# Kernel optimization log

Measured on AMD Instinct MI355X. Metric: run time of the kernel, lower is better.

The kernel has to match this reference:

```python
import jax, jax.numpy as jnp
import numpy as np

B, S, D, H = 4, 2048, 1024, 16
DK = D // H
INFTY = 1000000.0
INIT_SCALE = 1.2  # RandomUniform(-1.2, 1.2) kernel initializer


def setup_inputs() -> dict:
    key = jax.random.key(0)
    ks = jax.random.split(key, 6)
    x = jax.random.normal(ks[0], (B, S, D), dtype=jnp.float32)
    mask = jax.random.randint(ks[1], (B, S), 0, 2) == 1  # bool padding mask
    WQ = jax.random.uniform(ks[2], (D, D), jnp.float32, -INIT_SCALE, INIT_SCALE)
    WK = jax.random.uniform(ks[3], (D, D), jnp.float32, -INIT_SCALE, INIT_SCALE)
    WV = jax.random.uniform(ks[4], (D, D), jnp.float32, -INIT_SCALE, INIT_SCALE)
    WO = jax.random.uniform(ks[5], (D, D), jnp.float32, -INIT_SCALE, INIT_SCALE)
    return {"x": x, "mask": mask, "WQ": WQ, "WK": WK, "WV": WV, "WO": WO}


def reference(x, mask, WQ, WK, WV, WO):
    # Faithful reproduction of the layout: reshape to (B, S, d_key, n_heads)
    # then permute, matching K.reshape/K.permute_dimensions in the original.
    q = (x @ WQ).reshape(B, S, DK, H).transpose(0, 3, 1, 2)  # (B, H, S, DK)
    k = (x @ WK).reshape(B, S, DK, H).transpose(0, 3, 2, 1)  # (B, H, DK, S)
    score = jnp.matmul(q, k) / np.sqrt(DK)                   # (B, H, S, S)
    # additive key masking: score - (~mask)[B,1,1,S] * infinity
    inv_mask = (~mask).astype(x.dtype)
    score = score - inv_mask[:, None, None, :] * INFTY
    score = jax.nn.softmax(score, axis=-1)                   # att_dropout == 0
    v = (x @ WV).reshape(B, S, DK, H).transpose(0, 3, 1, 2)  # (B, H, S, DK)
    o = jnp.matmul(score, v)                                 # (B, H, S, DK)
    o = o.transpose(0, 2, 1, 3).reshape(B, S, H * DK)
    o = o @ WO                                               # (B, S, D)
    # final query-position masking + abs, as in the original
    o = jnp.abs(o * mask.astype(x.dtype)[:, :, None])
    return o
```

## Files before the change

### kernel.cpp

```cpp
#include <hip/hip_runtime.h>
#include <hip/hip_bf16.h>
#include <cstdint>
#include <cstddef>

constexpr int Bc  = 4;
constexpr int Sc  = 2048;
constexpr int Dc  = 1024;
constexpr int Hc  = 16;
constexpr int DKc = 64;
constexpr int Mtot = Bc * Sc;
constexpr float SC2  = 0.125f * 1.4426950408889634f;
constexpr float INF2 = 1000000.0f * 1.4426950408889634f;
constexpr float SXq  = 5400.0f;
constexpr float SWq  = 27166.0f;
constexpr float INVS = 1.0f / (SXq * SWq);

typedef short bf16x8 __attribute__((ext_vector_type(8)));
typedef float f32x4  __attribute__((ext_vector_type(4)));
typedef int   i32x4  __attribute__((ext_vector_type(4)));
typedef unsigned int u32x4 __attribute__((ext_vector_type(4)));

__device__ inline unsigned short bf16_rn(float f) {
    uint32_t u = __float_as_uint(f);
    uint32_t r = (u + 0x7FFFu + ((u >> 16) & 1u)) >> 16;
    return (unsigned short)r;
}
__device__ inline uint32_t pk_bf16(float a, float b) {
    uint32_t d;
    asm("v_cvt_pk_bf16_f32 %0, %1, %2" : "=v"(d) : "v"(a), "v"(b));
    return d;
}
__device__ inline int perm64(int k) {
    return (k & ~63) | (((k & 15) << 2) | ((k >> 4) & 3));
}
__device__ inline void mfma_i8(i32x4& acc, u32x4 a, u32x4 b) {
    asm volatile("v_mfma_i32_16x16x64_i8 %0, %1, %2, %0" : "+v"(acc) : "v"(a), "v"(b));
}
__device__ inline void split_i16(int fx, char& h, char& l) {
    int lo = ((fx + 128) & 255) - 128;
    h = (char)((fx - lo) >> 8);
    l = (char)lo;
}
__device__ inline void gl_lds16(const void* g, void* l) {
    __builtin_amdgcn_global_load_lds(
        (const __attribute__((address_space(1))) unsigned int*)g,
        (__attribute__((address_space(3))) unsigned int*)l, 16, 0, 0);
}

__global__ __launch_bounds__(256) void mask_norm(const void* __restrict__ mraw,
                                                 int* __restrict__ mi,
                                                 int* __restrict__ rinv,
                                                 int* __restrict__ nbv,
                                                 int* __restrict__ npadv) {
    __shared__ int fF32, fU8, fI32;
    __shared__ int part[256];
    __shared__ int nb_sh;
    if (threadIdx.x == 0) { fF32 = 0; fU8 = 0; fI32 = 0; }
    __syncthreads();
    const unsigned char* mb = (const unsigned char*)mraw;
    int aF = 0, a1 = 0, a4 = 0;
    for (int i = threadIdx.x; i < Mtot; i += 256) {
        unsigned char v = mb[i];
        if ((i & 3) == 3 && v == 0x3F) aF = 1;
        if (v) {
            if (i & 3) a1 = 1;
            else if (i & 7) a4 = 1;
        }
    }
    if (aF) fF32 = 1;
    if (a1) fU8 = 1;
    if (a4) fI32 = 1;
    __syncthreads();
    if (fF32) {
        const float* mf = (const float*)mraw;
        for (int s = threadIdx.x; s < Mtot; s += 256) mi[s] = (mf[s] != 0.0f);
    } else if (fU8) {
        for (int s = threadIdx.x; s < Mtot; s += 256) mi[s] = (mb[s] != 0);
    } else if (fI32) {
        const int* m32 = (const int*)mraw;
        for (int s = threadIdx.x; s < Mtot; s += 256) mi[s] = (m32[s] != 0);
    } else {
        const long long* m64 = (const long long*)mraw;
        for (int s = threadIdx.x; s < Mtot; s += 256) mi[s] = (m64[s] != 0);
    }
    __syncthreads();

    for (int b = 0; b < Bc; ++b) {
        const int* mrow = mi + b * Sc;
        int loc[8], cnt = 0;
        #pragma unroll
        for (int u = 0; u < 8; ++u) {
            loc[u] = mrow[threadIdx.x * 8 + u];
            cnt += loc[u];
        }
        part[threadIdx.x] = cnt;
        __syncthreads();
        if (threadIdx.x == 0) {
            int run = 0;
            for (int i = 0; i < 256; ++i) { int c = part[i]; part[i] = run; run += c; }
            nbv[b] = run;
            npadv[b] = (run + 63) & ~63;
            nb_sh = run;
        }
        __syncthreads();
        const int nbb = nb_sh;
        int pos = part[threadIdx.x];
        #pragma unroll
        for (int u = 0; u < 8; ++u) {
            const int s = threadIdx.x * 8 + u;
            if (loc[u]) {
                rinv[b * Sc + pos] = s;
                pos++;
            } else {
                rinv[b * Sc + nbb + (s - pos)] = s;
            }
        }
        __syncthreads();
    }
}

__global__ __launch_bounds__(256) void zero_pad(const int* __restrict__ nbv,
                                                const int* __restrict__ npadv,
                                                unsigned short* __restrict__ Khi,
                                                unsigned short* __restrict__ Klo,
                                                unsigned short* __restrict__ Vt) {
    const int bh = blockIdx.x;
    const int b = bh >> 4;
    const int nb = nbv[b], np = npadv[b];
    const int t = threadIdx.x;
    const size_t kbase = (size_t)bh * Sc * DKc;
    const size_t vbase = (size_t)bh * DKc * Sc;
    const int n = (np - nb) * DKc;
    for (int i = t; i < n; i += 256) {
        const int r = nb + i / DKc, c = i % DKc;
        Khi[kbase + (size_t)r * DKc + c] = 0;
        Klo[kbase + (size_t)r * DKc + c] = 0;
        Vt[vbase + (size_t)c * Sc + perm64(r)] = 0;
    }
}

__global__ __launch_bounds__(256) void quant_x(const float* __restrict__ x,
                                               unsigned short* __restrict__ xhi,
                                               signed char* __restrict__ xh8,
                                               signed char* __restrict__ xl8) {
    const int i = (blockIdx.x * 256 + threadIdx.x) * 4;
    float4 v = *reinterpret_cast<const float4*>(x + i);
    ushort4 hb;
    hb.x = bf16_rn(v.x); hb.y = bf16_rn(v.y); hb.z = bf16_rn(v.z); hb.w = bf16_rn(v.w);
    *reinterpret_cast<ushort4*>(xhi + i) = hb;
    char4 h8, l8;
    int fx;
    fx = min(max(__float2int_rn(v.x * SXq), -32640), 32640); split_i16(fx, h8.x, l8.x);
    fx = min(max(__float2int_rn(v.y * SXq), -32640), 32640); split_i16(fx, h8.y, l8.y);
    fx = min(max(__float2int_rn(v.z * SXq), -32640), 32640); split_i16(fx, h8.z, l8.z);
    fx = min(max(__float2int_rn(v.w * SXq), -32640), 32640); split_i16(fx, h8.w, l8.w);
    *reinterpret_cast<char4*>(xh8 + i) = h8;
    *reinterpret_cast<char4*>(xl8 + i) = l8;
}

template<bool PERM>
__global__ __launch_bounds__(256) void split_wt(const float* __restrict__ W,
                                                unsigned short* __restrict__ WhT) {
    __shared__ float ls[64][68];
    const int k0 = blockIdx.y * 64, n0 = blockIdx.x * 64;
    const int t = threadIdx.x;
    #pragma unroll
    for (int l = 0; l < 4; ++l) {
        const int idx = t + l * 256;
        const int r = idx >> 4, c = (idx & 15) * 4;
        *reinterpret_cast<float4*>(&ls[r][c]) =
            *reinterpret_cast<const float4*>(W + (size_t)(k0 + r) * Dc + n0 + c);
    }
    __syncthreads();
    #pragma unroll
    for (int l = 0; l < 4; ++l) {
        const int idx = t + l * 256;
        const int on = idx >> 4, kq = (idx & 15) * 4;
        #pragma unroll
        for (int j = 0; j < 4; ++j) {
            const float v = ls[kq + j][on];
            const int k  = k0 + kq + j;
            const int kd = PERM ? perm64(k) : k;
            WhT[(size_t)(n0 + on) * Dc + kd] = bf16_rn(v);
        }
    }
}

__global__ __launch_bounds__(256) void split_wt_i8(const float* __restrict__ W,
                                                   signed char* __restrict__ Wh8,
                                                   signed char* __restrict__ Wl8) {
    __shared__ float ls[64][68];
    const int k0 = blockIdx.y * 64, n0 = blockIdx.x * 64;
    const int t = threadIdx.x;
    #pragma unroll
    for (int l = 0; l < 4; ++l) {
        const int idx = t + l * 256;
        const int r = idx >> 4, c = (idx & 15) * 4;
        *reinterpret_cast<float4*>(&ls[r][c]) =
            *reinterpret_cast<const float4*>(W + (size_t)(k0 + r) * Dc + n0 + c);
    }
    __syncthreads();
    #pragma unroll
    for (int l = 0; l < 4; ++l) {
        const int idx = t + l * 256;
        const int on = idx >> 4, kq = (idx & 15) * 4;
        char4 hv, lv;
        int fx;
        fx = __float2int_rn(ls[kq + 0][on] * SWq); split_i16(fx, hv.x, lv.x);
        fx = __float2int_rn(ls[kq + 1][on] * SWq); split_i16(fx, hv.y, lv.y);
        fx = __float2int_rn(ls[kq + 2][on] * SWq); split_i16(fx, hv.z, lv.z);
        fx = __float2int_rn(ls[kq + 3][on] * SWq); split_i16(fx, hv.w, lv.w);
        const size_t o = (size_t)(n0 + on) * Dc + k0 + kq;
        *reinterpret_cast<char4*>(Wh8 + o) = hv;
        *reinterpret_cast<char4*>(Wl8 + o) = lv;
    }
}

__global__ __launch_bounds__(256) void gemm_i8qk(
    const signed char* __restrict__ Ah8, const signed char* __restrict__ Al8,
    const signed char* __restrict__ Bh8, const signed char* __restrict__ Bl8,
    const int* __restrict__ rinv, const int* __restrict__ nbv, float scale,
    unsigned short* __restrict__ O1, unsigned short* __restrict__ O2) {
    __shared__ __align__(16) signed char Ah[128 * 64];
    __shared__ __align__(16) signed char Al[128 * 64];
    __shared__ __align__(16) signed char Bh[128 * 64];
    __shared__ __align__(16) signed char Bl[128 * 64];
    const int t = threadIdx.x;
    const int n0 = blockIdx.x * 128, m0 = blockIdx.y * 128;
    const int b = m0 >> 11, mm0 = m0 & 2047;
    const int nb = nbv[b];
    if (mm0 >= nb) return;
    const int wv = t >> 6, lane = t & 63, li = lane & 15, lg = lane >> 4;
    const int wm = (wv >> 1) * 64, wn = (wv & 1) * 64;

    size_t gAr[2];
    int rowN[2];
    #pragma unroll
    for (int c = 0; c < 2; ++c) {
        const int ci  = wv * 2 + c;
        const int row = ci * 16 + (lane >> 2);
        rowN[c] = n0 + row;
        gAr[c] = ((size_t)b * Sc + rinv[b * Sc + mm0 + row]) * Dc;
    }
    const int cq = (lane & 3) * 16;

    i32x4 a1[4][4] = {};
    i32x4 a2[4][4] = {};
    asm volatile("s_nop 7" :::);

    for (int k0 = 0; k0 < Dc; k0 += 64) {
        __syncthreads();
        #pragma unroll
        for (int c = 0; c < 2; ++c) {
            const int ci = wv * 2 + c;
            const size_t ga = gAr[c] + k0 + cq;
            const size_t gb = (size_t)rowN[c] * Dc + k0 + cq;
            gl_lds16(Ah8 + ga, &Ah[ci * 1024]);
            gl_lds16(Al8 + ga, &Al[ci * 1024]);
            gl_lds16(Bh8 + gb, &Bh[ci * 1024]);
            gl_lds16(Bl8 + gb, &Bl[ci * 1024]);
        }
        __syncthreads();

        u32x4 bhf[4], blf[4];
        #pragma unroll
        for (int ni = 0; ni < 4; ++ni) {
            bhf[ni] = *reinterpret_cast<const u32x4*>(&Bh[(wn + ni * 16 + li) * 64 + lg * 16]);
            blf[ni] = *reinterpret_cast<const u32x4*>(&Bl[(wn + ni * 16 + li) * 64 + lg * 16]);
        }
        #pragma unroll
        for (int mi = 0; mi < 4; ++mi) {
            const u32x4 ahf = *reinterpret_cast<const u32x4*>(&Ah[(wm + mi * 16 + li) * 64 + lg * 16]);
            const u32x4 alf = *reinterpret_cast<const u32x4*>(&Al[(wm + mi * 16 + li) * 64 + lg * 16]);
            #pragma unroll
            for (int ni = 0; ni < 4; ++ni) {
                mfma_i8(a1[mi][ni], ahf, bhf[ni]);
                mfma_i8(a2[mi][ni], ahf, blf[ni]);
                mfma_i8(a2[mi][ni], alf, bhf[ni]);
            }
        }
    }

    asm volatile("s_nop 7\ns_nop 7\ns_nop 7" :::);

    #pragma unroll
    for (int mi = 0; mi < 4; ++mi) {
        #pragma unroll
        for (int r = 0; r < 4; ++r) {
            const int cs = mm0 + wm + mi * 16 + lg * 4 + r;
            if (cs >= nb) continue;
            #pragma unroll
            for (int ni = 0; ni < 4; ++ni) {
                const int n = n0 + wn + ni * 16 + li;
                const int h = n & 15, dk = n >> 4;
                const float f = fmaf((float)a1[mi][ni][r], 65536.0f,
                                     (float)a2[mi][ni][r] * 256.0f) * scale;
                const size_t o = ((size_t)(b * Hc + h) * Sc + cs) * DKc + dk;
                const unsigned short hi = bf16_rn(f);
                O1[o] = hi;
                O2[o] = bf16_rn(f - __uint_as_float((uint32_t)hi << 16));
            }
        }
    }
}

template<int EPI>
__global__ __launch_bounds__(256) void gemm_bf16(
    const unsigned short* __restrict__ Ahi,
    const unsigned short* __restrict__ Bhi,
    const int* __restrict__ rinv, const int* __restrict__ nbv,
    unsigned short* __restrict__ O1,
    float* __restrict__ Of) {
    __shared__ __align__(16) unsigned short Ah[128 * 32];
    __shared__ __align__(16) unsigned short Bh[128 * 32];
    const int t = threadIdx.x;
    const int n0 = blockIdx.x * 128, m0 = blockIdx.y * 128;
    const int b = m0 >> 11, mm0 = m0 & 2047;
    const int nb = nbv[b];
    const int wv = t >> 6, lane = t & 63, li = lane & 15, lg = lane >> 4;
    const int wm = (wv >> 1) * 64, wn = (wv & 1) * 64;

    if (EPI == 1 && mm0 >= nb) return;
    if (EPI == 2 && mm0 >= nb) {
        #pragma unroll
        for (int mi = 0; mi < 4; ++mi) {
            #pragma unroll
            for (int r = 0; r < 4; ++r) {
                const int cs = mm0 + wm + mi * 16 + lg * 4 + r;
                const int gs = rinv[b * Sc + cs];
                #pragma unroll
                for (int ni = 0; ni < 4; ++ni) {
                    const int n = n0 + wn + ni * 16 + li;
                    Of[((size_t)(b * Sc + gs)) * Dc + n] = 0.0f;
                }
            }
        }
        return;
    }

    size_t gAr[2];
    int rowN[2];
    #pragma unroll
    for (int c = 0; c < 2; ++c) {
        const int ci  = wv * 2 + c;
        const int row = ci * 16 + (lane >> 2);
        rowN[c] = n0 + row;
        if (EPI == 1)
            gAr[c] = ((size_t)b * Sc + rinv[b * Sc + mm0 + row]) * Dc;
        else
            gAr[c] = (size_t)(m0 + row) * Dc;
    }
    const int cq = (lane & 3) * 8;

    f32x4 acc[4][4] = {};

    for (int k0 = 0; k0 < Dc; k0 += 32) {
        __syncthreads();
        #pragma unroll
        for (int c = 0; c < 2; ++c) {
            const int ci = wv * 2 + c;
            gl_lds16(Ahi + gAr[c] + k0 + cq, &Ah[ci * 512]);
            gl_lds16(Bhi + (size_t)rowN[c] * Dc + k0 + cq, &Bh[ci * 512]);
        }
        __syncthreads();

        bf16x8 bhf[4];
        #pragma unroll
        for (int ni = 0; ni < 4; ++ni)
            bhf[ni] = *reinterpret_cast<const bf16x8*>(&Bh[(wn + ni * 16 + li) * 32 + lg * 8]);
        #pragma unroll
        for (int mi = 0; mi < 4; ++mi) {
            const bf16x8 ahf = *reinterpret_cast<const bf16x8*>(&Ah[(wm + mi * 16 + li) * 32 + lg * 8]);
            #pragma unroll
            for (int ni = 0; ni < 4; ++ni)
                acc[mi][ni] = __builtin_amdgcn_mfma_f32_16x16x32_bf16(ahf, bhf[ni], acc[mi][ni], 0, 0, 0);
        }
    }

    #pragma unroll
    for (int mi = 0; mi < 4; ++mi) {
        #pragma unroll
        for (int r = 0; r < 4; ++r) {
            const int cs = mm0 + wm + mi * 16 + lg * 4 + r;
            if (EPI == 1) {
                if (cs >= nb) continue;
                #pragma unroll
                for (int ni = 0; ni < 4; ++ni) {
                    const int n = n0 + wn + ni * 16 + li;
                    const int h = n & 15, dk = n >> 4;
                    O1[((size_t)(b * Hc + h) * DKc + dk) * Sc + perm64(cs)] =
                        bf16_rn(acc[mi][ni][r]);
                }
            } else {
                const int gs = rinv[b * Sc + cs];
                const bool valid = (cs < nb);
                #pragma unroll
                for (int ni = 0; ni < 4; ++ni) {
                    const int n = n0 + wn + ni * 16 + li;
                    Of[((size_t)(b * Sc + gs)) * Dc + n] =
                        valid ? fabsf(acc[mi][ni][r]) : 0.0f;
                }
            }
        }
    }
}

__global__ __launch_bounds__(512) void attn_mfma(const unsigned short* __restrict__ Qhi,
                                                 const unsigned short* __restrict__ Qlo,
                                                 const unsigned short* __restrict__ Khi,
                                                 const unsigned short* __restrict__ Klo,
                                                 const unsigned short* __restrict__ Vtg,
                                                 const int* __restrict__ nbv,
                                                 const int* __restrict__ npadv,
                                                 unsigned short* __restrict__ att) {
    constexpr int TK = 64;
    const int id  = blockIdx.x;
    const int swz = (id & 7) * 128 + (id >> 3);
    const int qb  = swz & 15;
    const int bh  = swz >> 4;
    const int b = bh >> 4, h = bh & 15;
    const int q0 = qb * 128;
    const int nb = nbv[b];
    if (q0 >= nb) return;
    const int ntile = npadv[b] >> 6;
    const int nt2 = (ntile + 1) >> 1;

    __shared__ __align__(16) unsigned short PsKs[2][128][72];
    __shared__ __align__(16) unsigned short Vs[2][80][72];

    const int t    = threadIdx.x;
    const int grp  = t >> 8;
    const int tg   = t & 255;
    const int wave = tg >> 6;
    const int lane = t & 63;
    const int lg   = lane >> 4;
    const int li   = lane & 15;

    const int myBase = grp ? nt2 : 0;
    const int myEnd  = grp ? ntile : nt2;

    {
        const int r = 64 + (tg >> 4), c4 = (tg & 15) * 4;
        const unsigned short val = ((tg >> 4) == 0) ? (unsigned short)0x3F80 : (unsigned short)0;
        ushort4 v; v.x = val; v.y = val; v.z = val; v.w = val;
        *reinterpret_cast<ushort4*>(&Vs[grp][r][c4]) = v;
    }

    bf16x8 qh[2][2], ql[2][2];
    #pragma unroll
    for (int hf = 0; hf < 2; ++hf) {
        const size_t qrow = ((size_t)bh * Sc + q0 + wave * 32 + hf * 16 + li) * DKc + lg * 8;
        qh[hf][0] = *reinterpret_cast<const bf16x8*>(Qhi + qrow);
        qh[hf][1] = *reinterpret_cast<const bf16x8*>(Qhi + qrow + 32);
        ql[hf][0] = *reinterpret_cast<const bf16x8*>(Qlo + qrow);
        ql[hf][1] = *reinterpret_cast<const bf16x8*>(Qlo + qrow + 32);
    }

    const size_t kbase = (size_t)bh * Sc * DKc;
    const size_t vbase = (size_t)bh * DKc * Sc;

    f32x4 accO[2][5] = {};
    float m[2][4];
    #pragma unroll
    for (int hf = 0; hf < 2; ++hf)
        #pragma unroll
        for (int r = 0; r < 4; ++r) m[hf][r] = -1e30f;

    for (int it = 0; it < nt2; ++it) {
        const int kt = myBase + it;
        const bool act = (kt < myEnd);
        const int k0 = kt * TK;
        __syncthreads();
        if (act) {
            #pragma unroll
            for (int u = 0; u < 2; ++u) {
                const int idx = tg + u * 256;
                const int r = idx >> 3, cc = (idx & 7) * 8;
                *reinterpret_cast<uint4*>(&PsKs[grp][r][cc]) =
                    *reinterpret_cast<const uint4*>(Khi + kbase + (size_t)(k0 + r) * DKc + cc);
                *reinterpret_cast<uint4*>(&PsKs[grp][64 + r][cc]) =
                    *reinterpret_cast<const uint4*>(Klo + kbase + (size_t)(k0 + r) * DKc + cc);
                *reinterpret_cast<uint4*>(&Vs[grp][r][cc]) =
                    *reinterpret_cast<const uint4*>(Vtg + vbase + (size_t)r * Sc + k0 + cc);
            }
        }
        __syncthreads();
        if (!act) continue;

        float sc[2][4][4];
        #pragma unroll
        for (int n = 0; n < 4; ++n) {
            const bf16x8 kh0 = *reinterpret_cast<const bf16x8*>(&PsKs[grp][n * 16 + li][lg * 8]);
            const bf16x8 kh1 = *reinterpret_cast<const bf16x8*>(&PsKs[grp][n * 16 + li][32 + lg * 8]);
            const bf16x8 kl0 = *reinterpret_cast<const bf16x8*>(&PsKs[grp][64 + n * 16 + li][lg * 8]);
            const bf16x8 kl1 = *reinterpret_cast<const bf16x8*>(&PsKs[grp][64 + n * 16 + li][32 + lg * 8]);
            const float mz = (k0 + n * 16 + li < nb) ? 0.0f : INF2;
            #pragma unroll
            for (int hf = 0; hf < 2; ++hf) {
                f32x4 a = {0, 0, 0, 0};
                a = __builtin_amdgcn_mfma_f32_16x16x32_bf16(qh[hf][0], kh0, a, 0, 0, 0);
                a = __builtin_amdgcn_mfma_f32_16x16x32_bf16(qh[hf][1], kh1, a, 0, 0, 0);
                a = __builtin_amdgcn_mfma_f32_16x16x32_bf16(qh[hf][0], kl0, a, 0, 0, 0);
                a = __builtin_amdgcn_mfma_f32_16x16x32_bf16(qh[hf][1], kl1, a, 0, 0, 0);
                a = __builtin_amdgcn_mfma_f32_16x16x32_bf16(ql[hf][0], kh0, a, 0, 0, 0);
                a = __builtin_amdgcn_mfma_f32_16x16x32_bf16(ql[hf][1], kh1, a, 0, 0, 0);
                #pragma unroll
                for (int r = 0; r < 4; ++r) sc[hf][n][r] = a[r] - mz;
            }
        }

        float mx[2][4], rs[2][4];
        #pragma unroll
        for (int hf = 0; hf < 2; ++hf)
            #pragma unroll
            for (int r = 0; r < 4; ++r)
                mx[hf][r] = fmaxf(fmaxf(sc[hf][0][r], sc[hf][1][r]),
                                  fmaxf(sc[hf][2][r], sc[hf][3][r]));
        #pragma unroll
        for (int o = 1; o < 16; o <<= 1)
            #pragma unroll
            for (int hf = 0; hf < 2; ++hf)
                #pragma unroll
                for (int r = 0; r < 4; ++r)
                    mx[hf][r] = fmaxf(mx[hf][r], __shfl_xor(mx[hf][r], o));
        #pragma unroll
        for (int hf = 0; hf < 2; ++hf)
            #pragma unroll
            for (int r = 0; r < 4; ++r) {
                const float mn = fmaxf(m[hf][r], mx[hf][r]);
                rs[hf][r] = exp2f(m[hf][r] - mn);
                m[hf][r]  = mn;
            }
        #pragma unroll
        for (int hf = 0; hf < 2; ++hf)
            #pragma unroll
            for (int r = 0; r < 4; ++r) {
                const float p0 = exp2f(sc[hf][0][r] - m[hf][r]);
                const float p1 = exp2f(sc[hf][1][r] - m[hf][r]);
                const float p2 = exp2f(sc[hf][2][r] - m[hf][r]);
                const float p3 = exp2f(sc[hf][3][r] - m[hf][r]);
                uint2 w;
                w.x = pk_bf16(p0, p1);
                w.y = pk_bf16(p2, p3);
                *reinterpret_cast<uint2*>(&PsKs[grp][wave * 32 + hf * 16 + lg * 4 + r][li * 4]) = w;
            }

        #pragma unroll
        for (int hf = 0; hf < 2; ++hf)
            #pragma unroll
            for (int dt = 0; dt < 5; ++dt)
                #pragma unroll
                for (int r = 0; r < 4; ++r)
                    accO[hf][dt][r] *= rs[hf][r];

        #pragma unroll
        for (int c = 0; c < 2; ++c) {
            bf16x8 pa[2];
            #pragma unroll
            for (int hf = 0; hf < 2; ++hf)
                pa[hf] = *reinterpret_cast<const bf16x8*>(&PsKs[grp][wave * 32 + hf * 16 + li][c * 32 + lg * 8]);
            #pragma unroll
            for (int dt = 0; dt < 5; ++dt) {
                const bf16x8 vb = *reinterpret_cast<const bf16x8*>(&Vs[grp][dt * 16 + li][c * 32 + lg * 8]);
                #pragma unroll
                for (int hf = 0; hf < 2; ++hf)
                    accO[hf][dt] = __builtin_amdgcn_mfma_f32_16x16x32_bf16(pa[hf], vb, accO[hf][dt], 0, 0, 0);
            }
        }
    }

    __syncthreads();
    float* pO  = (float*)&PsKs[0][0][0];
    float* pML = pO + 128 * 64;

    if (grp == 1) {
        #pragma unroll
        for (int hf = 0; hf < 2; ++hf) {
            #pragma unroll
            for (int r = 0; r < 4; ++r) {
                const int row = wave * 32 + hf * 16 + lg * 4 + r;
                if (li == 0) {
                    pML[row * 2]     = m[hf][r];
                    pML[row * 2 + 1] = accO[hf][4][r];
                }
                float4 o = make_float4(accO[hf][0][r], accO[hf][1][r],
                                       accO[hf][2][r], accO[hf][3][r]);
                *reinterpret_cast<float4*>(&pO[row * 64 + li * 4]) = o;
            }
        }
    }
    __syncthreads();
    if (grp == 0) {
        #pragma unroll
        for (int hf = 0; hf < 2; ++hf) {
            #pragma unroll
            for (int r = 0; r < 4; ++r) {
                const int row = wave * 32 + hf * 16 + lg * 4 + r;
                const float m1 = pML[row * 2];
                const float l1 = pML[row * 2 + 1];
                const float l0 = __shfl(accO[hf][4][r], lane & 0x30);
                const float ms = fmaxf(m[hf][r], m1);
                const float s0 = exp2f(m[hf][r] - ms);
                const float s1 = exp2f(m1 - ms);
                const float inv = 1.0f / (l0 * s0 + l1 * s1);
                const float4 o1 = *reinterpret_cast<const float4*>(&pO[row * 64 + li * 4]);
                const int q = q0 + row;
                uint2 w;
                w.x = pk_bf16((accO[hf][0][r] * s0 + o1.x * s1) * inv,
                              (accO[hf][1][r] * s0 + o1.y * s1) * inv);
                w.y = pk_bf16((accO[hf][2][r] * s0 + o1.z * s1) * inv,
                              (accO[hf][3][r] * s0 + o1.w * s1) * inv);
                *reinterpret_cast<uint2*>(att + (size_t)(b * Sc + q) * Dc + h * DKc + li * 4) = w;
            }
        }
    }
}

extern "C" void kernel_launch(void* const* d_in, const int* in_sizes, int n_in,
                              void* d_out, int out_size, void* d_ws, size_t ws_size,
                              hipStream_t stream) {
    const float* x    = (const float*)d_in[0];
    const void*  mraw = d_in[1];
    const float* WQ   = (const float*)d_in[2];
    const float* WK   = (const float*)d_in[3];
    const float* WV   = (const float*)d_in[4];
    const float* WO   = (const float*)d_in[5];
    float* out = (float*)d_out;

    int* mi    = (int*)d_ws;
    int* rinv  = mi + Mtot;
    int* nbv   = rinv + Mtot;
    int* npadv = nbv + 4;
    const size_t SZ = (size_t)Mtot * Dc;
    const size_t WSZ = (size_t)Dc * Dc;
    char* p = (char*)d_ws + 65664;
    unsigned short* xhi = (unsigned short*)p;            p += SZ * 2;
    signed char*    xh8 = (signed char*)p;               p += SZ;
    signed char*    xl8 = (signed char*)p;               p += SZ;
    unsigned short* WVh = (unsigned short*)p;            p += WSZ * 2;
    unsigned short* WOh = (unsigned short*)p;            p += WSZ * 2;
    signed char*    WQh8 = (signed char*)p;              p += WSZ;
    signed char*    WQl8 = (signed char*)p;              p += WSZ;
    signed char*    WKh8 = (signed char*)p;              p += WSZ;
    signed char*    WKl8 = (signed char*)p;              p += WSZ;
    unsigned short* Qhi = (unsigned short*)p;            p += SZ * 2;
    unsigned short* Qlo = (unsigned short*)p;            p += SZ * 2;
    unsigned short* Khi = (unsigned short*)p;            p += SZ * 2;
    unsigned short* Klo = (unsigned short*)p;            p += SZ * 2;
    unsigned short* Vt  = (unsigned short*)p;            p += SZ * 2;
    unsigned short* att = xhi;

    mask_norm<<<1, 256, 0, stream>>>(mraw, mi, rinv, nbv, npadv);
    quant_x<<<(int)(SZ / 1024), 256, 0, stream>>>(x, xhi, xh8, xl8);
    const dim3 gW(16, 16);
    split_wt_i8<<<gW, 256, 0, stream>>>(WQ, WQh8, WQl8);
    split_wt_i8<<<gW, 256, 0, stream>>>(WK, WKh8, WKl8);
    split_wt<false><<<gW, 256, 0, stream>>>(WV, WVh);
    split_wt<true ><<<gW, 256, 0, stream>>>(WO, WOh);
    zero_pad<<<dim3(64), 256, 0, stream>>>(nbv, npadv, Khi, Klo, Vt);

    const dim3 gG(Dc / 128, Mtot / 128);
    gemm_i8qk<<<gG, 256, 0, stream>>>(xh8, xl8, WQh8, WQl8, rinv, nbv, SC2 * INVS, Qhi, Qlo);
    gemm_i8qk<<<gG, 256, 0, stream>>>(xh8, xl8, WKh8, WKl8, rinv, nbv, INVS, Khi, Klo);
    gemm_bf16<1><<<gG, 256, 0, stream>>>(xhi, WVh, rinv, nbv, Vt, nullptr);

    attn_mfma<<<dim3(1024), 512, 0, stream>>>(Qhi, Qlo, Khi, Klo, Vt, nbv, npadv, att);

    gemm_bf16<2><<<gG, 256, 0, stream>>>(att, WOh, rinv, nbv, nullptr, out);
}
```

Baseline: 305.5 us.

## Fuse Q, K, V projections into one int8 split-precision GEMM launch

The V projection moves from the bf16 GEMM to the same int8 hi/lo split GEMM used for Q and K. All three weight matrices are concatenated into one buffer and computed by a single launch with 24 column tiles, and each tile picks its output tensor and scale from its column range. This drops the bf16 copy of x, the separate bf16 V weight, and two kernel launches, and it gives better occupancy through one larger grid. In exchange V now costs three int8 MFMAs per step instead of one bf16 MFMA. The V epilogue also changes to the int8 scaling and rounding path.

After: 321.2 us. +5.1%, slower.

```diff
diff --git a/kernel.cpp b/kernel.cpp
--- a/kernel.cpp
+++ b/kernel.cpp
@@ -140,14 +140,10 @@
 }
 
 __global__ __launch_bounds__(256) void quant_x(const float* __restrict__ x,
-                                               unsigned short* __restrict__ xhi,
                                                signed char* __restrict__ xh8,
                                                signed char* __restrict__ xl8) {
     const int i = (blockIdx.x * 256 + threadIdx.x) * 4;
     float4 v = *reinterpret_cast<const float4*>(x + i);
-    ushort4 hb;
-    hb.x = bf16_rn(v.x); hb.y = bf16_rn(v.y); hb.z = bf16_rn(v.z); hb.w = bf16_rn(v.w);
-    *reinterpret_cast<ushort4*>(xhi + i) = hb;
     char4 h8, l8;
     int fx;
     fx = min(max(__float2int_rn(v.x * SXq), -32640), 32640); split_i16(fx, h8.x, l8.x);
@@ -158,9 +154,8 @@
     *reinterpret_cast<char4*>(xl8 + i) = l8;
 }
 
-template<bool PERM>
-__global__ __launch_bounds__(256) void split_wt(const float* __restrict__ W,
-                                                unsigned short* __restrict__ WhT) {
+__global__ __launch_bounds__(256) void split_wt_o(const float* __restrict__ W,
+                                                  unsigned short* __restrict__ WhT) {
     __shared__ float ls[64][68];
     const int k0 = blockIdx.y * 64, n0 = blockIdx.x * 64;
     const int t = threadIdx.x;
@@ -179,8 +174,7 @@
         #pragma unroll
         for (int j = 0; j < 4; ++j) {
             const float v = ls[kq + j][on];
-            const int k  = k0 + kq + j;
-            const int kd = PERM ? perm64(k) : k;
+            const int kd = perm64(k0 + kq + j);
             WhT[(size_t)(n0 + on) * Dc + kd] = bf16_rn(v);
         }
     }
@@ -216,11 +210,13 @@
     }
 }
 
-__global__ __launch_bounds__(256) void gemm_i8qk(
+__global__ __launch_bounds__(256) void gemm_i8qkv(
     const signed char* __restrict__ Ah8, const signed char* __restrict__ Al8,
     const signed char* __restrict__ Bh8, const signed char* __restrict__ Bl8,
-    const int* __restrict__ rinv, const int* __restrict__ nbv, float scale,
-    unsigned short* __restrict__ O1, unsigned short* __restrict__ O2) {
+    const int* __restrict__ rinv, const int* __restrict__ nbv,
+    unsigned short* __restrict__ Qhi, unsigned short* __restrict__ Qlo,
+    unsigned short* __restrict__ Khi, unsigned short* __restrict__ Klo,
+    unsigned short* __restrict__ Vt) {
     __shared__ __align__(16) signed char Ah[128 * 64];
     __shared__ __align__(16) signed char Al[128 * 64];
     __shared__ __align__(16) signed char Bh[128 * 64];
@@ -283,6 +279,11 @@
 
     asm volatile("s_nop 7\ns_nop 7\ns_nop 7" :::);
 
+    const int sel = n0 >> 10;
+    const float scale = (sel == 0) ? (SC2 * INVS) : INVS;
+    unsigned short* O1 = (sel == 0) ? Qhi : Khi;
+    unsigned short* O2 = (sel == 0) ? Qlo : Klo;
+
     #pragma unroll
     for (int mi = 0; mi < 4; ++mi) {
         #pragma unroll
@@ -292,24 +293,27 @@
             #pragma unroll
             for (int ni = 0; ni < 4; ++ni) {
                 const int n = n0 + wn + ni * 16 + li;
-                const int h = n & 15, dk = n >> 4;
+                const int nn = n & 1023;
+                const int h = nn & 15, dk = nn >> 4;
                 const float f = fmaf((float)a1[mi][ni][r], 65536.0f,
                                      (float)a2[mi][ni][r] * 256.0f) * scale;
-                const size_t o = ((size_t)(b * Hc + h) * Sc + cs) * DKc + dk;
-                const unsigned short hi = bf16_rn(f);
-                O1[o] = hi;
-                O2[o] = bf16_rn(f - __uint_as_float((uint32_t)hi << 16));
-            }
-        }
-    }
-}
-
-template<int EPI>
-__global__ __launch_bounds__(256) void gemm_bf16(
+                if (sel < 2) {
+                    const size_t o = ((size_t)(b * Hc + h) * Sc + cs) * DKc + dk;
+                    const unsigned short hi = bf16_rn(f);
+                    O1[o] = hi;
+                    O2[o] = bf16_rn(f - __uint_as_float((uint32_t)hi << 16));
+                } else {
+                    Vt[((size_t)(b * Hc + h) * DKc + dk) * Sc + perm64(cs)] = bf16_rn(f);
+                }
+            }
+        }
+    }
+}
+
+__global__ __launch_bounds__(256) void gemm_oproj(
     const unsigned short* __restrict__ Ahi,
     const unsigned short* __restrict__ Bhi,
     const int* __restrict__ rinv, const int* __restrict__ nbv,
-    unsigned short* __restrict__ O1,
     float* __restrict__ Of) {
     __shared__ __align__(16) unsigned short Ah[128 * 32];
     __shared__ __align__(16) unsigned short Bh[128 * 32];
@@ -320,8 +324,7 @@
     const int wv = t >> 6, lane = t & 63, li = lane & 15, lg = lane >> 4;
     const int wm = (wv >> 1) * 64, wn = (wv & 1) * 64;
 
-    if (EPI == 1 && mm0 >= nb) return;
-    if (EPI == 2 && mm0 >= nb) {
+    if (mm0 >= nb) {
         #pragma unroll
         for (int mi = 0; mi < 4; ++mi) {
             #pragma unroll
@@ -338,29 +341,17 @@
         return;
     }
 
-    size_t gAr[2];
-    int rowN[2];
-    #pragma unroll
-    for (int c = 0; c < 2; ++c) {
-        const int ci  = wv * 2 + c;
-        const int row = ci * 16 + (lane >> 2);
-        rowN[c] = n0 + row;
-        if (EPI == 1)
-            gAr[c] = ((size_t)b * Sc + rinv[b * Sc + mm0 + row]) * Dc;
-        else
-            gAr[c] = (size_t)(m0 + row) * Dc;
-    }
-    const int cq = (lane & 3) * 8;
-
     f32x4 acc[4][4] = {};
 
     for (int k0 = 0; k0 < Dc; k0 += 32) {
         __syncthreads();
         #pragma unroll
         for (int c = 0; c < 2; ++c) {
-            const int ci = wv * 2 + c;
-            gl_lds16(Ahi + gAr[c] + k0 + cq, &Ah[ci * 512]);
-            gl_lds16(Bhi + (size_t)rowN[c] * Dc + k0 + cq, &Bh[ci * 512]);
+            const int ci  = wv * 2 + c;
+            const int row = ci * 16 + (lane >> 2);
+            const int cq  = (lane & 3) * 8;
+            gl_lds16(Ahi + (size_t)(m0 + row) * Dc + k0 + cq, &Ah[ci * 512]);
+            gl_lds16(Bhi + (size_t)(n0 + row) * Dc + k0 + cq, &Bh[ci * 512]);
         }
         __syncthreads();
 
@@ -382,24 +373,13 @@
         #pragma unroll
         for (int r = 0; r < 4; ++r) {
             const int cs = mm0 + wm + mi * 16 + lg * 4 + r;
-            if (EPI == 1) {
-                if (cs >= nb) continue;
-                #pragma unroll
-                for (int ni = 0; ni < 4; ++ni) {
-                    const int n = n0 + wn + ni * 16 + li;
-                    const int h = n & 15, dk = n >> 4;
-                    O1[((size_t)(b * Hc + h) * DKc + dk) * Sc + perm64(cs)] =
-                        bf16_rn(acc[mi][ni][r]);
-                }
-            } else {
-                const int gs = rinv[b * Sc + cs];
-                const bool valid = (cs < nb);
-                #pragma unroll
-                for (int ni = 0; ni < 4; ++ni) {
-                    const int n = n0 + wn + ni * 16 + li;
-                    Of[((size_t)(b * Sc + gs)) * Dc + n] =
-                        valid ? fabsf(acc[mi][ni][r]) : 0.0f;
-                }
+            const int gs = rinv[b * Sc + cs];
+            const bool valid = (cs < nb);
+            #pragma unroll
+            for (int ni = 0; ni < 4; ++ni) {
+                const int n = n0 + wn + ni * 16 + li;
+                Of[((size_t)(b * Sc + gs)) * Dc + n] =
+                    valid ? fabsf(acc[mi][ni][r]) : 0.0f;
             }
         }
     }
@@ -634,37 +614,31 @@
     const size_t SZ = (size_t)Mtot * Dc;
     const size_t WSZ = (size_t)Dc * Dc;
     char* p = (char*)d_ws + 65664;
-    unsigned short* xhi = (unsigned short*)p;            p += SZ * 2;
     signed char*    xh8 = (signed char*)p;               p += SZ;
     signed char*    xl8 = (signed char*)p;               p += SZ;
-    unsigned short* WVh = (unsigned short*)p;            p += WSZ * 2;
     unsigned short* WOh = (unsigned short*)p;            p += WSZ * 2;
-    signed char*    WQh8 = (signed char*)p;              p += WSZ;
-    signed char*    WQl8 = (signed char*)p;              p += WSZ;
-    signed char*    WKh8 = (signed char*)p;              p += WSZ;
-    signed char*    WKl8 = (signed char*)p;              p += WSZ;
+    signed char*    Wqkvh8 = (signed char*)p;            p += 3 * WSZ;
+    signed char*    Wqkvl8 = (signed char*)p;            p += 3 * WSZ;
     unsigned short* Qhi = (unsigned short*)p;            p += SZ * 2;
     unsigned short* Qlo = (unsigned short*)p;            p += SZ * 2;
     unsigned short* Khi = (unsigned short*)p;            p += SZ * 2;
     unsigned short* Klo = (unsigned short*)p;            p += SZ * 2;
     unsigned short* Vt  = (unsigned short*)p;            p += SZ * 2;
-    unsigned short* att = xhi;
+    unsigned short* att = (unsigned short*)xh8;
 
     mask_norm<<<1, 256, 0, stream>>>(mraw, mi, rinv, nbv, npadv);
-    quant_x<<<(int)(SZ / 1024), 256, 0, stream>>>(x, xhi, xh8, xl8);
+    quant_x<<<(int)(SZ / 1024), 256, 0, stream>>>(x, xh8, xl8);
     const dim3 gW(16, 16);
-    split_wt_i8<<<gW, 256, 0, stream>>>(WQ, WQh8, WQl8);
-    split_wt_i8<<<gW, 256, 0, stream>>>(WK, WKh8, WKl8);
-    split_wt<false><<<gW, 256, 0, stream>>>(WV, WVh);
-    split_wt<true ><<<gW, 256, 0, stream>>>(WO, WOh);
+    split_wt_i8<<<gW, 256, 0, stream>>>(WQ, Wqkvh8, Wqkvl8);
+    split_wt_i8<<<gW, 256, 0, stream>>>(WK, Wqkvh8 + WSZ, Wqkvl8 + WSZ);
+    split_wt_i8<<<gW, 256, 0, stream>>>(WV, Wqkvh8 + 2 * WSZ, Wqkvl8 + 2 * WSZ);
+    split_wt_o<<<gW, 256, 0, stream>>>(WO, WOh);
     zero_pad<<<dim3(64), 256, 0, stream>>>(nbv, npadv, Khi, Klo, Vt);
 
-    const dim3 gG(Dc / 128, Mtot / 128);
-    gemm_i8qk<<<gG, 256, 0, stream>>>(xh8, xl8, WQh8, WQl8, rinv, nbv, SC2 * INVS, Qhi, Qlo);
-    gemm_i8qk<<<gG, 256, 0, stream>>>(xh8, xl8, WKh8, WKl8, rinv, nbv, INVS, Khi, Klo);
-    gemm_bf16<1><<<gG, 256, 0, stream>>>(xhi, WVh, rinv, nbv, Vt, nullptr);
+    gemm_i8qkv<<<dim3(24, 64), 256, 0, stream>>>(xh8, xl8, Wqkvh8, Wqkvl8,
+                                                 rinv, nbv, Qhi, Qlo, Khi, Klo, Vt);
 
     attn_mfma<<<dim3(1024), 512, 0, stream>>>(Qhi, Qlo, Khi, Klo, Vt, nbv, npadv, att);
 
-    gemm_bf16<2><<<gG, 256, 0, stream>>>(att, WOh, rinv, nbv, nullptr, out);
-}
+    gemm_oproj<<<dim3(8, 64), 256, 0, stream>>>(att, WOh, rinv, nbv, out);
+}
```

## Vectorize Q/K and V-transpose epilogue stores and drop V key permutation

Applied to the files above, without the earlier changes.

Changes the output layouts so the QK projection epilogue writes four consecutive dk values per head as one ushort4 store, and the V-transpose epilogue writes four consecutive sequence positions as one ushort4. To make this work, the perm64 key permutation on V is removed, and the P tile written to shared memory in attention is scattered into column slots li, li+16, li+32, li+48 instead of a packed uint2. This keeps the P column order consistent with the unpermuted V. The aim is fewer, wider global stores in the projection epilogues, paid for with four scalar LDS writes per row in the attention inner loop. It also relies on the unseen attention and layout code agreeing with the new channel and head ordering.

Result: faster. 298.8 us (-2.2%).

```diff
diff --git a/kernel.cpp b/kernel.cpp
--- a/kernel.cpp
+++ b/kernel.cpp
@@ -135,7 +135,7 @@
         const int r = nb + i / DKc, c = i % DKc;
         Khi[kbase + (size_t)r * DKc + c] = 0;
         Klo[kbase + (size_t)r * DKc + c] = 0;
-        Vt[vbase + (size_t)c * Sc + perm64(r)] = 0;
+        Vt[vbase + (size_t)c * Sc + r] = 0;
     }
 }
 
@@ -283,23 +283,28 @@
 
     asm volatile("s_nop 7\ns_nop 7\ns_nop 7" :::);
 
+    const int dkb = (n0 + wn) >> 4;
     #pragma unroll
     for (int mi = 0; mi < 4; ++mi) {
         #pragma unroll
         for (int r = 0; r < 4; ++r) {
             const int cs = mm0 + wm + mi * 16 + lg * 4 + r;
             if (cs >= nb) continue;
-            #pragma unroll
-            for (int ni = 0; ni < 4; ++ni) {
-                const int n = n0 + wn + ni * 16 + li;
-                const int h = n & 15, dk = n >> 4;
-                const float f = fmaf((float)a1[mi][ni][r], 65536.0f,
-                                     (float)a2[mi][ni][r] * 256.0f) * scale;
-                const size_t o = ((size_t)(b * Hc + h) * Sc + cs) * DKc + dk;
-                const unsigned short hi = bf16_rn(f);
-                O1[o] = hi;
-                O2[o] = bf16_rn(f - __uint_as_float((uint32_t)hi << 16));
-            }
+            const size_t ob = ((size_t)(b * Hc + li) * Sc + cs) * DKc + dkb;
+            ushort4 hq, lq;
+            float fv[4];
+            #pragma unroll
+            for (int ni = 0; ni < 4; ++ni)
+                fv[ni] = fmaf((float)a1[mi][ni][r], 65536.0f,
+                              (float)a2[mi][ni][r] * 256.0f) * scale;
+            hq.x = bf16_rn(fv[0]); hq.y = bf16_rn(fv[1]);
+            hq.z = bf16_rn(fv[2]); hq.w = bf16_rn(fv[3]);
+            lq.x = bf16_rn(fv[0] - __uint_as_float((uint32_t)hq.x << 16));
+            lq.y = bf16_rn(fv[1] - __uint_as_float((uint32_t)hq.y << 16));
+            lq.z = bf16_rn(fv[2] - __uint_as_float((uint32_t)hq.z << 16));
+            lq.w = bf16_rn(fv[3] - __uint_as_float((uint32_t)hq.w << 16));
+            *reinterpret_cast<ushort4*>(O1 + ob) = hq;
+            *reinterpret_cast<ushort4*>(O2 + ob) = lq;
         }
     }
 }
@@ -379,19 +384,30 @@
 
     #pragma unroll
     for (int mi = 0; mi < 4; ++mi) {
-        #pragma unroll
-        for (int r = 0; r < 4; ++r) {
-            const int cs = mm0 + wm + mi * 16 + lg * 4 + r;
-            if (EPI == 1) {
-                if (cs >= nb) continue;
-                #pragma unroll
-                for (int ni = 0; ni < 4; ++ni) {
-                    const int n = n0 + wn + ni * 16 + li;
-                    const int h = n & 15, dk = n >> 4;
-                    O1[((size_t)(b * Hc + h) * DKc + dk) * Sc + perm64(cs)] =
-                        bf16_rn(acc[mi][ni][r]);
+        if (EPI == 1) {
+            const int csb = mm0 + wm + mi * 16 + lg * 4;
+            #pragma unroll
+            for (int ni = 0; ni < 4; ++ni) {
+                const int n = n0 + wn + ni * 16 + li;
+                const int h = n & 15, dk = n >> 4;
+                const size_t ob = ((size_t)(b * Hc + h) * DKc + dk) * Sc + csb;
+                if (csb + 3 < nb) {
+                    ushort4 vq;
+                    vq.x = bf16_rn(acc[mi][ni][0]);
+                    vq.y = bf16_rn(acc[mi][ni][1]);
+                    vq.z = bf16_rn(acc[mi][ni][2]);
+                    vq.w = bf16_rn(acc[mi][ni][3]);
+                    *reinterpret_cast<ushort4*>(O1 + ob) = vq;
+                } else {
+                    #pragma unroll
+                    for (int r = 0; r < 4; ++r)
+                        if (csb + r < nb) O1[ob + r] = bf16_rn(acc[mi][ni][r]);
                 }
-            } else {
+            }
+        } else {
+            #pragma unroll
+            for (int r = 0; r < 4; ++r) {
+                const int cs = mm0 + wm + mi * 16 + lg * 4 + r;
                 const int gs = rinv[b * Sc + cs];
                 const bool valid = (cs < nb);
                 #pragma unroll
@@ -535,14 +551,15 @@
         for (int hf = 0; hf < 2; ++hf)
             #pragma unroll
             for (int r = 0; r < 4; ++r) {
-                const float p0 = exp2f(sc[hf][0][r] - m[hf][r]);
-                const float p1 = exp2f(sc[hf][1][r] - m[hf][r]);
-                const float p2 = exp2f(sc[hf][2][r] - m[hf][r]);
-                const float p3 = exp2f(sc[hf][3][r] - m[hf][r]);
-                uint2 w;
-                w.x = pk_bf16(p0, p1);
-                w.y = pk_bf16(p2, p3);
-                *reinterpret_cast<uint2*>(&PsKs[grp][wave * 32 + hf * 16 + lg * 4 + r][li * 4]) = w;
+                const int row = wave * 32 + hf * 16 + lg * 4 + r;
+                const uint32_t w01 = pk_bf16(exp2f(sc[hf][0][r] - m[hf][r]),
+                                             exp2f(sc[hf][1][r] - m[hf][r]));
+                const uint32_t w23 = pk_bf16(exp2f(sc[hf][2][r] - m[hf][r]),
+                                             exp2f(sc[hf][3][r] - m[hf][r]));
+                PsKs[grp][row][li]      = (unsigned short)w01;
+                PsKs[grp][row][li + 16] = (unsigned short)(w01 >> 16);
+                PsKs[grp][row][li + 32] = (unsigned short)w23;
+                PsKs[grp][row][li + 48] = (unsigned short)(w23 >> 16);
             }
 
         #pragma unroll
```
